# Optimization experiments

Measured on AMD Instinct MI355X. Metric: run time of the kernel, lower is better.

The kernel has to match this reference:

```python
import jax, jax.numpy as jnp
import numpy as np

N_NODES = 100000
N_FEAT = 128
N_HID = 256
N_REL = 3
N_EDGE = 400000
N_PAIR = 200000


def setup_inputs() -> dict:
    key = jax.random.key(0)
    ks = jax.random.split(key, 8)
    x = jax.random.normal(ks[0], (N_NODES, N_FEAT), jnp.float32)
    edge_src = jax.random.randint(ks[1], (N_REL, N_EDGE), 0, N_NODES, jnp.int32)
    edge_dst = jax.random.randint(ks[2], (N_REL, N_EDGE), 0, N_NODES, jnp.int32)
    edge_mask = jnp.ones((N_REL, N_EDGE), bool)
    n_pairs = jax.random.randint(ks[3], (N_PAIR, 2), 0, N_NODES, jnp.int32)
    W1 = jax.random.normal(ks[4], (N_REL, N_FEAT, N_HID), jnp.float32) / np.sqrt(N_FEAT).astype(np.float32)
    b1 = jnp.zeros((N_REL, N_HID), jnp.float32)
    W2 = jax.random.normal(ks[5], (N_REL, N_HID, N_FEAT), jnp.float32) / np.sqrt(N_HID).astype(np.float32)
    b2 = jnp.zeros((N_REL, N_FEAT), jnp.float32)
    linW = jax.random.normal(ks[6], (2 * N_FEAT, 1), jnp.float32) / np.sqrt(2 * N_FEAT).astype(np.float32)
    linb = jnp.zeros((1,), jnp.float32)
    return dict(x=x, edge_src=edge_src, edge_dst=edge_dst, edge_mask=edge_mask,
                n_pairs=n_pairs, W1=W1, b1=b1, W2=W2, b2=b2, linW=linW, linb=linb)


def graph_conv(x, W, b, src, dst):
    # DGL GraphConv, norm='both': D_dst^{-1/2} A D_src^{-1/2} X W + b
    n = x.shape[0]
    ones = jnp.ones(src.shape, x.dtype)
    deg_out = jnp.maximum(jax.ops.segment_sum(ones, src, num_segments=n), 1.0)
    deg_in = jnp.maximum(jax.ops.segment_sum(ones, dst, num_segments=n), 1.0)
    h = (x * (deg_out ** -0.5)[:, None]) @ W           # [N, out]
    agg = jax.ops.segment_sum(h[src], dst, num_segments=n)  # SpMM
    return agg * (deg_in ** -0.5)[:, None] + b


def reference(x, edge_src, edge_dst, edge_mask, n_pairs, W1, b1, W2, b2, linW, linb):
    def hetero_layer(feat, W, b):
        # one GraphConv per relation, HeteroGraphConv aggregate='mean'
        outs = jax.vmap(lambda s, d, w, bb: graph_conv(feat, w, bb, s, d))(edge_src, edge_dst, W, b)
        return outs.mean(0)

    h = jax.nn.relu(hetero_layer(x, W1, b1))   # [N, H]
    h = hetero_layer(h, W2, b2)                # [N, F]
    # per-edge-type src/dst gather + concat; edge_mask is all-True so boolean
    # selection is the identity and the row count stays static
    pe = jnp.concatenate([h[edge_src], h[edge_dst]], axis=-1)   # [R, E, 2F]
    pe = pe.reshape(-1, 2 * h.shape[1])
    pp = jnp.concatenate([h[n_pairs[:, 0]], h[n_pairs[:, 1]]], axis=1)  # [P, 2F]
    feats = jnp.concatenate([pe, pp], axis=0)
    return jax.nn.sigmoid(jax.nn.relu(feats) @ linW + linb)
```

## Files before the change

kernel.cpp:

```cpp
#include <hip/hip_runtime.h>
#include <math.h>

#define NND  100000
#define NNDP 100096
#define NF   128
#define NH   256
#define NR   3
#define NE   400000
#define NP   200000

#define SCHUNK 2048
#define SCAN_N (NR * NNDP)
#define SBLOCKS ((SCAN_N + SCHUNK - 1) / SCHUNK)

typedef __attribute__((ext_vector_type(8))) short bf16x8;
typedef __attribute__((ext_vector_type(8))) unsigned short u16x8;
typedef __attribute__((ext_vector_type(4))) float f32x4;

static __device__ __forceinline__ unsigned short f2bf(float f) {
    unsigned u = __float_as_uint(f);
    unsigned r = (u + 0x7fffu + ((u >> 16) & 1u)) >> 16;
    return (unsigned short)r;
}
static __device__ __forceinline__ float bf2f(unsigned short h) {
    return __uint_as_float(((unsigned)h) << 16);
}

__global__ void degree_kernel(const int* __restrict__ esrc, const int* __restrict__ edst,
                              int* __restrict__ dout, int* __restrict__ din) {
    int gid = blockIdx.x * blockDim.x + threadIdx.x;
    if (gid >= NR * NE) return;
    int r = gid / NE;
    atomicAdd(dout + (size_t)r * NNDP + esrc[gid], 1);
    atomicAdd(din  + (size_t)r * NNDP + edst[gid], 1);
}

__global__ void norm_finalize(const int* __restrict__ deg, float* __restrict__ nrm, int n) {
    int gid = blockIdx.x * blockDim.x + threadIdx.x;
    if (gid < n) {
        float v = (float)deg[gid];
        nrm[gid] = 1.f / sqrtf(fmaxf(v, 1.f));
    }
}

__global__ void scan1(const int* __restrict__ in, int* __restrict__ out, int* __restrict__ bsum) {
    __shared__ int sm[256];
    int t = threadIdx.x;
    int base = blockIdx.x * SCHUNK + t * 8;
    int v[8];
    int tsum = 0;
#pragma unroll
    for (int i = 0; i < 8; ++i) {
        v[i] = (base + i < SCAN_N) ? in[base + i] : 0;
        tsum += v[i];
    }
    sm[t] = tsum;
    __syncthreads();
    for (int off = 1; off < 256; off <<= 1) {
        int tv = (t >= off) ? sm[t - off] : 0;
        __syncthreads();
        sm[t] += tv;
        __syncthreads();
    }
    int excl = sm[t] - tsum;
    if (t == 255) bsum[blockIdx.x] = sm[255];
    int run = excl;
#pragma unroll
    for (int i = 0; i < 8; ++i) {
        if (base + i < SCAN_N) out[base + i] = run;
        run += v[i];
    }
}

__global__ void scan2(int* __restrict__ bsum) {
    __shared__ int sm[256];
    int t = threadIdx.x;
    int v = (t < SBLOCKS) ? bsum[t] : 0;
    sm[t] = v;
    __syncthreads();
    for (int off = 1; off < 256; off <<= 1) {
        int tv = (t >= off) ? sm[t - off] : 0;
        __syncthreads();
        sm[t] += tv;
        __syncthreads();
    }
    if (t < SBLOCKS) bsum[t] = sm[t] - v;
}

__global__ void scan3(int* __restrict__ out, const int* __restrict__ bsum) {
    int gid = blockIdx.x * blockDim.x + threadIdx.x;
    if (gid < SCAN_N) out[gid] += bsum[gid / SCHUNK];
}

__global__ void csr_fill(const int* __restrict__ esrc, const int* __restrict__ edst,
                         const int* __restrict__ rp, int* __restrict__ cursor,
                         int* __restrict__ csr) {
    int gid = blockIdx.x * blockDim.x + threadIdx.x;
    if (gid >= NR * NE) return;
    int r = gid / NE;
    int g = r * NNDP + edst[gid];
    int pos = atomicAdd(&cursor[g], 1);
    csr[rp[g] + pos] = esrc[gid];
}

__global__ void prep_w1(const float* __restrict__ W1,
                        unsigned short* __restrict__ Wh, unsigned short* __restrict__ Wl) {
    int idx = blockIdx.x * blockDim.x + threadIdx.x;
    if (idx >= NR * NF * NH) return;
    int r = idx / (NF * NH);
    int rem = idx % (NF * NH);
    int k = rem >> 8;
    int n = rem & 255;
    float v = W1[idx];
    unsigned short h = f2bf(v);
    size_t o = ((size_t)r * NH + n) * NF + k;
    Wh[o] = h;
    Wl[o] = f2bf(v - bf2f(h));
}

__global__ void prep_w2(const float* __restrict__ W2,
                        unsigned short* __restrict__ Wh, unsigned short* __restrict__ Wl) {
    int idx = blockIdx.x * blockDim.x + threadIdx.x;
    if (idx >= NR * NH * NF) return;
    int r = idx / (NH * NF);
    int rem = idx % (NH * NF);
    int k = rem >> 7;
    int j = rem & 127;
    float v = W2[idx];
    unsigned short h = f2bf(v);
    size_t o = ((size_t)r * NF + j) * NH + k;
    Wh[o] = h;
    Wl[o] = f2bf(v - bf2f(h));
}

__global__ void prep_bias(const float* __restrict__ b1, float* __restrict__ bmean) {
    int j = blockIdx.x * blockDim.x + threadIdx.x;
    if (j < NH) bmean[j] = (b1[j] + b1[NH + j] + b1[2 * NH + j]) * (1.f / 3.f);
}

__launch_bounds__(256)
__global__ void layer1_fused(const float* __restrict__ x,
                             const int* __restrict__ rp, const int* __restrict__ deg,
                             const int* __restrict__ csr,
                             const float* __restrict__ nrm_out, const float* __restrict__ nrm_in,
                             const unsigned short* __restrict__ W1h, const unsigned short* __restrict__ W1l,
                             const float* __restrict__ bmean,
                             unsigned short* __restrict__ h1h, unsigned short* __restrict__ h1l) {
    constexpr int AP = 136;
    __shared__ unsigned short As_h[64 * AP];
    __shared__ unsigned short As_l[64 * AP];

    const int tid = threadIdx.x;
    const int lane = tid & 63;
    const int wv = tid >> 6;
    const int lr = lane & 15;
    const int lg = lane >> 4;
    const int m0 = blockIdx.x * 64;
    const int cb = wv * 64;

    f32x4 acc[4][4];
    const f32x4 z = {0.f, 0.f, 0.f, 0.f};
#pragma unroll
    for (int a = 0; a < 4; ++a)
#pragma unroll
        for (int b = 0; b < 4; ++b) acc[a][b] = z;

    const int arow = tid >> 2;
    const int fch = (tid & 3) << 5;

    for (int r = 0; r < NR; ++r) {
        const int g = r * NNDP + m0 + arow;
        const int p0 = rp[g];
        const int cnt = deg[g];
        const float* no = nrm_out + (size_t)r * NNDP;
        float a[32];
#pragma unroll
        for (int i = 0; i < 32; ++i) a[i] = 0.f;
        for (int e = 0; e < cnt; ++e) {
            int s = csr[p0 + e];
            float sc = no[s];
            const float4* xp = reinterpret_cast<const float4*>(x + (size_t)s * NF + fch);
#pragma unroll
            for (int v = 0; v < 8; ++v) {
                float4 q = xp[v];
                a[v * 4 + 0] += q.x * sc;
                a[v * 4 + 1] += q.y * sc;
                a[v * 4 + 2] += q.z * sc;
                a[v * 4 + 3] += q.w * sc;
            }
        }
        const float di = nrm_in[g];
#pragma unroll
        for (int v = 0; v < 4; ++v) {
            u16x8 hv, lv;
#pragma unroll
            for (int i = 0; i < 8; ++i) {
                float val = a[v * 8 + i] * di;
                unsigned short h = f2bf(val);
                hv[i] = h;
                lv[i] = f2bf(val - bf2f(h));
            }
            int off = arow * AP + fch + v * 8;
            *reinterpret_cast<u16x8*>(&As_h[off]) = hv;
            *reinterpret_cast<u16x8*>(&As_l[off]) = lv;
        }
        __syncthreads();

        const unsigned short* Bh = W1h + (size_t)r * NH * NF;
        const unsigned short* Bl = W1l + (size_t)r * NH * NF;
#pragma unroll
        for (int ks = 0; ks < 4; ++ks) {
            bf16x8 a_h[4], a_l[4], b_h[4], b_l[4];
#pragma unroll
            for (int f = 0; f < 4; ++f) {
                int ao = (f * 16 + lr) * AP + ks * 32 + lg * 8;
                a_h[f] = *reinterpret_cast<const bf16x8*>(&As_h[ao]);
                a_l[f] = *reinterpret_cast<const bf16x8*>(&As_l[ao]);
                size_t bo = (size_t)(cb + f * 16 + lr) * NF + ks * 32 + lg * 8;
                b_h[f] = *reinterpret_cast<const bf16x8*>(Bh + bo);
                b_l[f] = *reinterpret_cast<const bf16x8*>(Bl + bo);
            }
#pragma unroll
            for (int fm = 0; fm < 4; ++fm)
#pragma unroll
                for (int fn = 0; fn < 4; ++fn) {
                    acc[fm][fn] = __builtin_amdgcn_mfma_f32_16x16x32_bf16(a_h[fm], b_h[fn], acc[fm][fn], 0, 0, 0);
                    acc[fm][fn] = __builtin_amdgcn_mfma_f32_16x16x32_bf16(a_h[fm], b_l[fn], acc[fm][fn], 0, 0, 0);
                    acc[fm][fn] = __builtin_amdgcn_mfma_f32_16x16x32_bf16(a_l[fm], b_h[fn], acc[fm][fn], 0, 0, 0);
                }
        }
        __syncthreads();
    }

    const float inv3 = 1.f / 3.f;
#pragma unroll
    for (int fm = 0; fm < 4; ++fm)
#pragma unroll
        for (int fn = 0; fn < 4; ++fn) {
            int col = cb + fn * 16 + lr;
            float bm = bmean[col];
#pragma unroll
            for (int j = 0; j < 4; ++j) {
                int row = m0 + fm * 16 + lg * 4 + j;
                float v = fmaxf(acc[fm][fn][j] * inv3 + bm, 0.f);
                unsigned short h = f2bf(v);
                size_t o = (size_t)row * NH + col;
                h1h[o] = h;
                h1l[o] = f2bf(v - bf2f(h));
            }
        }
}

__launch_bounds__(256)
__global__ void gemm2_mfma(const unsigned short* __restrict__ Ah, const unsigned short* __restrict__ Al,
                           const unsigned short* __restrict__ Bh, const unsigned short* __restrict__ Bl,
                           const float* __restrict__ nrm_out_r,
                           float* __restrict__ C) {
    const int lane = threadIdx.x & 63;
    const int wv = threadIdx.x >> 6;
    const int lr = lane & 15;
    const int lg = lane >> 4;
    const int m0 = blockIdx.x * 64;
    const int cb = wv * 32;

    f32x4 acc[4][2];
    const f32x4 z = {0.f, 0.f, 0.f, 0.f};
#pragma unroll
    for (int a = 0; a < 4; ++a)
#pragma unroll
        for (int b = 0; b < 2; ++b) acc[a][b] = z;

    const size_t aoff = (size_t)(m0 + lr) * NH + lg * 8;
    const size_t boff = (size_t)(cb + lr) * NH + lg * 8;

#pragma unroll
    for (int ks = 0; ks < 8; ++ks) {
        bf16x8 a_h[4], a_l[4], b_h[2], b_l[2];
#pragma unroll
        for (int f = 0; f < 4; ++f) {
            size_t ao = aoff + (size_t)f * 16 * NH + ks * 32;
            a_h[f] = *reinterpret_cast<const bf16x8*>(Ah + ao);
            a_l[f] = *reinterpret_cast<const bf16x8*>(Al + ao);
        }
#pragma unroll
        for (int f = 0; f < 2; ++f) {
            size_t bo = boff + (size_t)f * 16 * NH + ks * 32;
            b_h[f] = *reinterpret_cast<const bf16x8*>(Bh + bo);
            b_l[f] = *reinterpret_cast<const bf16x8*>(Bl + bo);
        }
#pragma unroll
        for (int fm = 0; fm < 4; ++fm)
#pragma unroll
            for (int fn = 0; fn < 2; ++fn) {
                acc[fm][fn] = __builtin_amdgcn_mfma_f32_16x16x32_bf16(a_h[fm], b_h[fn], acc[fm][fn], 0, 0, 0);
                acc[fm][fn] = __builtin_amdgcn_mfma_f32_16x16x32_bf16(a_h[fm], b_l[fn], acc[fm][fn], 0, 0, 0);
                acc[fm][fn] = __builtin_amdgcn_mfma_f32_16x16x32_bf16(a_l[fm], b_h[fn], acc[fm][fn], 0, 0, 0);
            }
    }

#pragma unroll
    for (int fm = 0; fm < 4; ++fm)
#pragma unroll
        for (int fn = 0; fn < 2; ++fn) {
            int col = cb + fn * 16 + lr;
#pragma unroll
            for (int j = 0; j < 4; ++j) {
                int row = m0 + fm * 16 + lg * 4 + j;
                C[(size_t)row * NF + col] = acc[fm][fn][j] * nrm_out_r[row];
            }
        }
}

template<bool ACCUM>
__launch_bounds__(256)
__global__ void agg2_gather(const float* __restrict__ C, float* __restrict__ h2,
                            const int* __restrict__ rp, const int* __restrict__ deg,
                            const int* __restrict__ csr, const float* __restrict__ nrm_in,
                            int rbase) {
    int tid = blockIdx.x * blockDim.x + threadIdx.x;
    int n = tid >> 6;
    int lane = tid & 63;
    if (n >= NNDP) return;
    int g = rbase + n;
    int p0 = rp[g];
    int cnt = deg[g];
    float ax = 0.f, ay = 0.f;
    for (int i = 0; i < cnt; ++i) {
        int s = csr[p0 + i];
        float2 v = *reinterpret_cast<const float2*>(C + (size_t)s * NF + lane * 2);
        ax += v.x;
        ay += v.y;
    }
    float sc = nrm_in[g];
    ax *= sc;
    ay *= sc;
    float* op = h2 + (size_t)n * NF + lane * 2;
    if (ACCUM) {
        ax += op[0];
        ay += op[1];
    }
    op[0] = ax;
    op[1] = ay;
}

__launch_bounds__(256)
__global__ void node_score(const float* __restrict__ h2, const float* __restrict__ b2,
                           const float* __restrict__ linW,
                           float* __restrict__ sa, float* __restrict__ sb) {
    int gid = blockIdx.x * blockDim.x + threadIdx.x;
    int n = gid >> 6;
    int lane = gid & 63;
    if (n >= NND) return;
    int k = lane * 2;
    float2 h = *reinterpret_cast<const float2*>(h2 + (size_t)n * NF + k);
    const float inv3 = 1.f / 3.f;
    float bm0 = (b2[k]     + b2[NF + k]     + b2[2 * NF + k])     * inv3;
    float bm1 = (b2[k + 1] + b2[NF + k + 1] + b2[2 * NF + k + 1]) * inv3;
    float v0 = fmaxf(h.x * inv3 + bm0, 0.f);
    float v1 = fmaxf(h.y * inv3 + bm1, 0.f);
    float pa = v0 * linW[k] + v1 * linW[k + 1];
    float pb = v0 * linW[NF + k] + v1 * linW[NF + k + 1];
#pragma unroll
    for (int off = 32; off; off >>= 1) {
        pa += __shfl_xor(pa, off);
        pb += __shfl_xor(pb, off);
    }
    if (lane == 0) {
        sa[n] = pa;
        sb[n] = pb;
    }
}

__global__ void pair_out(const float* __restrict__ sa, const float* __restrict__ sb,
                         const int* __restrict__ esrc, const int* __restrict__ edst,
                         const int* __restrict__ pairs, const float* __restrict__ linb,
                         float* __restrict__ out) {
    int i = blockIdx.x * blockDim.x + threadIdx.x;
    const int TE = NR * NE;
    if (i >= TE + NP) return;
    int s, d;
    if (i < TE) {
        s = esrc[i];
        d = edst[i];
    } else {
        int p = i - TE;
        s = pairs[2 * p];
        d = pairs[2 * p + 1];
    }
    float z = sa[s] + sb[d] + linb[0];
    out[i] = 1.f / (1.f + expf(-z));
}

extern "C" void kernel_launch(void* const* d_in, const int* in_sizes, int n_in,
                              void* d_out, int out_size, void* d_ws, size_t ws_size,
                              hipStream_t stream) {
    const float* x    = (const float*)d_in[0];
    const int*   esrc = (const int*)d_in[1];
    const int*   edst = (const int*)d_in[2];
    const int*   prs  = (const int*)d_in[4];
    const float* W1   = (const float*)d_in[5];
    const float* b1   = (const float*)d_in[6];
    const float* W2   = (const float*)d_in[7];
    const float* b2   = (const float*)d_in[8];
    const float* linW = (const float*)d_in[9];
    const float* linb = (const float*)d_in[10];
    float* out = (float*)d_out;

    char* ws = (char*)d_ws;
    size_t off = 0;
    auto alloc = [&](size_t bytes) -> void* {
        void* p = ws + off;
        off += (bytes + 255) & ~(size_t)255;
        return p;
    };
    int*   deg_out_i = (int*)alloc((size_t)SCAN_N * 4);
    int*   deg_in_i  = (int*)alloc((size_t)SCAN_N * 4);
    float* norm_out  = (float*)alloc((size_t)SCAN_N * 4);
    float* norm_in   = (float*)alloc((size_t)SCAN_N * 4);
    int*   row_ptr   = (int*)alloc((size_t)SCAN_N * 4);
    int*   bsum      = (int*)alloc((size_t)SBLOCKS * 4);
    int*   csr       = (int*)alloc((size_t)NR * NE * 4);
    unsigned short* Wt1h = (unsigned short*)alloc((size_t)NR * NH * NF * 2);
    unsigned short* Wt1l = (unsigned short*)alloc((size_t)NR * NH * NF * 2);
    unsigned short* Wt2h = (unsigned short*)alloc((size_t)NR * NF * NH * 2);
    unsigned short* Wt2l = (unsigned short*)alloc((size_t)NR * NF * NH * 2);
    float* bmean = (float*)alloc((size_t)NH * 4);
    float* sa    = (float*)alloc((size_t)NNDP * 4);
    float* sb    = (float*)alloc((size_t)NNDP * 4);

    unsigned short* h1h = (unsigned short*)alloc((size_t)NNDP * NH * 2);
    unsigned short* h1l = (unsigned short*)alloc((size_t)NNDP * NH * 2);
    float* c2 = (float*)alloc((size_t)NNDP * NF * 4);
    float* h2 = (float*)alloc((size_t)NNDP * NF * 4);
    int* cursor = deg_out_i;

    hipMemsetAsync(deg_out_i, 0, (size_t)SCAN_N * 4, stream);
    hipMemsetAsync(deg_in_i,  0, (size_t)SCAN_N * 4, stream);

    degree_kernel<<<(NR * NE + 255) / 256, 256, 0, stream>>>(esrc, edst, deg_out_i, deg_in_i);
    norm_finalize<<<(SCAN_N + 255) / 256, 256, 0, stream>>>(deg_out_i, norm_out, SCAN_N);
    norm_finalize<<<(SCAN_N + 255) / 256, 256, 0, stream>>>(deg_in_i, norm_in, SCAN_N);

    scan1<<<SBLOCKS, 256, 0, stream>>>(deg_in_i, row_ptr, bsum);
    scan2<<<1, 256, 0, stream>>>(bsum);
    scan3<<<(SCAN_N + 255) / 256, 256, 0, stream>>>(row_ptr, bsum);
    hipMemsetAsync(cursor, 0, (size_t)SCAN_N * 4, stream);
    csr_fill<<<(NR * NE + 255) / 256, 256, 0, stream>>>(esrc, edst, row_ptr, cursor, csr);

    prep_w1<<<(NR * NF * NH + 255) / 256, 256, 0, stream>>>(W1, Wt1h, Wt1l);
    prep_w2<<<(NR * NH * NF + 255) / 256, 256, 0, stream>>>(W2, Wt2h, Wt2l);
    prep_bias<<<1, 256, 0, stream>>>(b1, bmean);

    layer1_fused<<<NNDP / 64, 256, 0, stream>>>(
        x, row_ptr, deg_in_i, csr, norm_out, norm_in, Wt1h, Wt1l, bmean, h1h, h1l);

    for (int r = 0; r < NR; ++r) {
        gemm2_mfma<<<NNDP / 64, 256, 0, stream>>>(
            h1h, h1l, Wt2h + (size_t)r * NF * NH, Wt2l + (size_t)r * NF * NH,
            norm_out + (size_t)r * NNDP, c2);
        if (r == 0)
            agg2_gather<false><<<NNDP * 64 / 256, 256, 0, stream>>>(
                c2, h2, row_ptr, deg_in_i, csr, norm_in, r * NNDP);
        else
            agg2_gather<true><<<NNDP * 64 / 256, 256, 0, stream>>>(
                c2, h2, row_ptr, deg_in_i, csr, norm_in, r * NNDP);
    }

    node_score<<<NND * 64 / 256, 256, 0, stream>>>(h2, b2, linW, sa, sb);
    pair_out<<<(NR * NE + NP + 255) / 256, 256, 0, stream>>>(sa, sb, esrc, edst, prs, linb, out);
}
```

Measured before the change: 970.9 us.

## Record CSR slots during degree count, swizzle LDS, unroll gathers

The degree kernel now stores the atomicAdd return value as each edge's slot, so csr_fill writes directly without a second atomic pass or a cursor memset. Layer 1's A tile in LDS switches from a padded layout to an XOR swizzle. The layer-1 neighbour gather processes two edges per iteration and the layer-2 gather processes four, to put more loads in flight. This adds an extra 4.8 MB epos buffer and more registers per thread.

```diff
diff --git a/kernel.cpp b/kernel.cpp
--- a/kernel.cpp
+++ b/kernel.cpp
@@ -27,12 +27,14 @@
 }
 
 __global__ void degree_kernel(const int* __restrict__ esrc, const int* __restrict__ edst,
-                              int* __restrict__ dout, int* __restrict__ din) {
+                              int* __restrict__ dout, int* __restrict__ din,
+                              int* __restrict__ epos) {
     int gid = blockIdx.x * blockDim.x + threadIdx.x;
     if (gid >= NR * NE) return;
     int r = gid / NE;
     atomicAdd(dout + (size_t)r * NNDP + esrc[gid], 1);
-    atomicAdd(din  + (size_t)r * NNDP + edst[gid], 1);
+    int pos = atomicAdd(din + (size_t)r * NNDP + edst[gid], 1);
+    epos[gid] = pos;
 }
 
 __global__ void norm_finalize(const int* __restrict__ deg, float* __restrict__ nrm, int n) {
@@ -93,14 +95,13 @@
 }
 
 __global__ void csr_fill(const int* __restrict__ esrc, const int* __restrict__ edst,
-                         const int* __restrict__ rp, int* __restrict__ cursor,
+                         const int* __restrict__ rp, const int* __restrict__ epos,
                          int* __restrict__ csr) {
     int gid = blockIdx.x * blockDim.x + threadIdx.x;
     if (gid >= NR * NE) return;
     int r = gid / NE;
     int g = r * NNDP + edst[gid];
-    int pos = atomicAdd(&cursor[g], 1);
-    csr[rp[g] + pos] = esrc[gid];
+    csr[rp[g] + epos[gid]] = esrc[gid];
 }
 
 __global__ void prep_w1(const float* __restrict__ W1,
@@ -138,6 +139,10 @@
     if (j < NH) bmean[j] = (b1[j] + b1[NH + j] + b1[2 * NH + j]) * (1.f / 3.f);
 }
 
+static __device__ __forceinline__ int lds_swz(int row, int col_shorts) {
+    return row * 128 + (col_shorts ^ ((row & 7) << 3));
+}
+
 __launch_bounds__(256)
 __global__ void layer1_fused(const float* __restrict__ x,
                              const int* __restrict__ rp, const int* __restrict__ deg,
@@ -146,9 +151,8 @@
                              const unsigned short* __restrict__ W1h, const unsigned short* __restrict__ W1l,
                              const float* __restrict__ bmean,
                              unsigned short* __restrict__ h1h, unsigned short* __restrict__ h1l) {
-    constexpr int AP = 136;
-    __shared__ unsigned short As_h[64 * AP];
-    __shared__ unsigned short As_l[64 * AP];
+    __shared__ unsigned short As_h[64 * 128];
+    __shared__ unsigned short As_l[64 * 128];
 
     const int tid = threadIdx.x;
     const int lane = tid & 63;
@@ -173,34 +177,60 @@
         const int p0 = rp[g];
         const int cnt = deg[g];
         const float* no = nrm_out + (size_t)r * NNDP;
-        float a[32];
-#pragma unroll
-        for (int i = 0; i < 32; ++i) a[i] = 0.f;
-        for (int e = 0; e < cnt; ++e) {
-            int s = csr[p0 + e];
-            float sc = no[s];
-            const float4* xp = reinterpret_cast<const float4*>(x + (size_t)s * NF + fch);
+        float4 ac[8];
+#pragma unroll
+        for (int i = 0; i < 8; ++i) ac[i] = make_float4(0.f, 0.f, 0.f, 0.f);
+
+        int e = 0;
+        for (; e + 2 <= cnt; e += 2) {
+            int s0 = csr[p0 + e];
+            int s1 = csr[p0 + e + 1];
+            float c0 = no[s0];
+            float c1 = no[s1];
+            const float4* xp0 = reinterpret_cast<const float4*>(x + (size_t)s0 * NF + fch);
+            const float4* xp1 = reinterpret_cast<const float4*>(x + (size_t)s1 * NF + fch);
+            float4 q0[8], q1[8];
+#pragma unroll
+            for (int v = 0; v < 8; ++v) q0[v] = xp0[v];
+#pragma unroll
+            for (int v = 0; v < 8; ++v) q1[v] = xp1[v];
 #pragma unroll
             for (int v = 0; v < 8; ++v) {
-                float4 q = xp[v];
-                a[v * 4 + 0] += q.x * sc;
-                a[v * 4 + 1] += q.y * sc;
-                a[v * 4 + 2] += q.z * sc;
-                a[v * 4 + 3] += q.w * sc;
-            }
-        }
+                ac[v].x += q0[v].x * c0 + q1[v].x * c1;
+                ac[v].y += q0[v].y * c0 + q1[v].y * c1;
+                ac[v].z += q0[v].z * c0 + q1[v].z * c1;
+                ac[v].w += q0[v].w * c0 + q1[v].w * c1;
+            }
+        }
+        if (e < cnt) {
+            int s0 = csr[p0 + e];
+            float c0 = no[s0];
+            const float4* xp0 = reinterpret_cast<const float4*>(x + (size_t)s0 * NF + fch);
+            float4 q0[8];
+#pragma unroll
+            for (int v = 0; v < 8; ++v) q0[v] = xp0[v];
+#pragma unroll
+            for (int v = 0; v < 8; ++v) {
+                ac[v].x += q0[v].x * c0;
+                ac[v].y += q0[v].y * c0;
+                ac[v].z += q0[v].z * c0;
+                ac[v].w += q0[v].w * c0;
+            }
+        }
+
         const float di = nrm_in[g];
 #pragma unroll
         for (int v = 0; v < 4; ++v) {
             u16x8 hv, lv;
+            float vals[8] = {ac[v*2].x * di, ac[v*2].y * di, ac[v*2].z * di, ac[v*2].w * di,
+                             ac[v*2+1].x * di, ac[v*2+1].y * di, ac[v*2+1].z * di, ac[v*2+1].w * di};
 #pragma unroll
             for (int i = 0; i < 8; ++i) {
-                float val = a[v * 8 + i] * di;
-                unsigned short h = f2bf(val);
+                unsigned short h = f2bf(vals[i]);
                 hv[i] = h;
-                lv[i] = f2bf(val - bf2f(h));
-            }
-            int off = arow * AP + fch + v * 8;
+                lv[i] = f2bf(vals[i] - bf2f(h));
+            }
+            int off = lds_swz(arow, fch + v * 8);
             *reinterpret_cast<u16x8*>(&As_h[off]) = hv;
             *reinterpret_cast<u16x8*>(&As_l[off]) = lv;
         }
@@ -213,7 +243,7 @@
             bf16x8 a_h[4], a_l[4], b_h[4], b_l[4];
 #pragma unroll
             for (int f = 0; f < 4; ++f) {
-                int ao = (f * 16 + lr) * AP + ks * 32 + lg * 8;
+                int ao = lds_swz(f * 16 + lr, ks * 32 + lg * 8);
                 a_h[f] = *reinterpret_cast<const bf16x8*>(&As_h[ao]);
                 a_l[f] = *reinterpret_cast<const bf16x8*>(&As_l[ao]);
                 size_t bo = (size_t)(cb + f * 16 + lr) * NF + ks * 32 + lg * 8;
@@ -325,7 +355,20 @@
     int p0 = rp[g];
     int cnt = deg[g];
     float ax = 0.f, ay = 0.f;
-    for (int i = 0; i < cnt; ++i) {
+    int i = 0;
+    for (; i + 4 <= cnt; i += 4) {
+        int s0 = csr[p0 + i];
+        int s1 = csr[p0 + i + 1];
+        int s2 = csr[p0 + i + 2];
+        int s3 = csr[p0 + i + 3];
+        float2 v0 = *reinterpret_cast<const float2*>(C + (size_t)s0 * NF + lane * 2);
+        float2 v1 = *reinterpret_cast<const float2*>(C + (size_t)s1 * NF + lane * 2);
+        float2 v2 = *reinterpret_cast<const float2*>(C + (size_t)s2 * NF + lane * 2);
+        float2 v3 = *reinterpret_cast<const float2*>(C + (size_t)s3 * NF + lane * 2);
+        ax += (v0.x + v1.x) + (v2.x + v3.x);
+        ay += (v0.y + v1.y) + (v2.y + v3.y);
+    }
+    for (; i < cnt; ++i) {
         int s = csr[p0 + i];
         float2 v = *reinterpret_cast<const float2*>(C + (size_t)s * NF + lane * 2);
         ax += v.x;
@@ -420,6 +463,7 @@
     int*   row_ptr   = (int*)alloc((size_t)SCAN_N * 4);
     int*   bsum      = (int*)alloc((size_t)SBLOCKS * 4);
     int*   csr       = (int*)alloc((size_t)NR * NE * 4);
+    int*   epos      = (int*)alloc((size_t)NR * NE * 4);
     unsigned short* Wt1h = (unsigned short*)alloc((size_t)NR * NH * NF * 2);
     unsigned short* Wt1l = (unsigned short*)alloc((size_t)NR * NH * NF * 2);
     unsigned short* Wt2h = (unsigned short*)alloc((size_t)NR * NF * NH * 2);
@@ -432,20 +476,18 @@
     unsigned short* h1l = (unsigned short*)alloc((size_t)NNDP * NH * 2);
     float* c2 = (float*)alloc((size_t)NNDP * NF * 4);
     float* h2 = (float*)alloc((size_t)NNDP * NF * 4);
-    int* cursor = deg_out_i;
 
     hipMemsetAsync(deg_out_i, 0, (size_t)SCAN_N * 4, stream);
     hipMemsetAsync(deg_in_i,  0, (size_t)SCAN_N * 4, stream);
 
-    degree_kernel<<<(NR * NE + 255) / 256, 256, 0, stream>>>(esrc, edst, deg_out_i, deg_in_i);
+    degree_kernel<<<(NR * NE + 255) / 256, 256, 0, stream>>>(esrc, edst, deg_out_i, deg_in_i, epos);
     norm_finalize<<<(SCAN_N + 255) / 256, 256, 0, stream>>>(deg_out_i, norm_out, SCAN_N);
     norm_finalize<<<(SCAN_N + 255) / 256, 256, 0, stream>>>(deg_in_i, norm_in, SCAN_N);
 
     scan1<<<SBLOCKS, 256, 0, stream>>>(deg_in_i, row_ptr, bsum);
     scan2<<<1, 256, 0, stream>>>(bsum);
     scan3<<<(SCAN_N + 255) / 256, 256, 0, stream>>>(row_ptr, bsum);
-    hipMemsetAsync(cursor, 0, (size_t)SCAN_N * 4, stream);
-    csr_fill<<<(NR * NE + 255) / 256, 256, 0, stream>>>(esrc, edst, row_ptr, cursor, csr);
+    csr_fill<<<(NR * NE + 255) / 256, 256, 0, stream>>>(esrc, edst, row_ptr, epos, csr);
 
     prep_w1<<<(NR * NF * NH + 255) / 256, 256, 0, stream>>>(W1, Wt1h, Wt1l);
     prep_w2<<<(NR * NH * NF + 255) / 256, 256, 0, stream>>>(W2, Wt2h, Wt2l);
```

Measured after the change: 888.3 us. 1.09x faster.
